# Performance work log

Measured on AMD Instinct MI355X. Metric: run time of the kernel, lower is better.

The kernel has to match this reference:

```python
import jax, jax.numpy as jnp
import numpy as np

D_FEAT = 6
T = 60
H = 64          # hidden_size
N = 8192        # number of stocks (cross-sectional batch)
LRELU_SLOPE = 0.01
BN_EPS = 1e-5


def _gru_layer(x_seq, W_ih, W_hh, b_ih, b_hh):
    """torch-convention GRU layer. x_seq: (N, T, in) -> (N, T, H)."""
    # precompute input projections for all timesteps: (N, T, 3H)
    xw = jnp.einsum('nti,gi->ntg', x_seq, W_ih) + b_ih

    def step(h, xt):
        gh = h @ W_hh.T + b_hh
        xr, xz, xn = jnp.split(xt, 3, axis=-1)
        hr, hz, hn = jnp.split(gh, 3, axis=-1)
        r = jax.nn.sigmoid(xr + hr)
        z = jax.nn.sigmoid(xz + hz)
        n = jnp.tanh(xn + r * hn)
        h_new = (1.0 - z) * n + z * h
        return h_new, h_new

    h0 = jnp.zeros((x_seq.shape[0], H), x_seq.dtype)
    _, ys = jax.lax.scan(step, h0, jnp.swapaxes(xw, 0, 1))  # (T, N, H)
    return jnp.swapaxes(ys, 0, 1)


def _batchnorm(x, w, b):
    # track_running_stats=False -> always batch statistics (biased var)
    m = jnp.mean(x, axis=0)
    v = jnp.var(x, axis=0)
    return (x - m) * jax.lax.rsqrt(v + BN_EPS) * w + b


def setup_inputs() -> dict:
    key = jax.random.key(0)
    ks = jax.random.split(key, 24)
    s = 1.0 / np.sqrt(H)

    def u(k, shape):
        return jax.random.uniform(k, shape, jnp.float32, -s, s)

    inp = {"x": jax.random.normal(ks[0], (N, D_FEAT * T), jnp.float32)}
    in_sizes = [D_FEAT, H]
    for l in range(2):
        inp[f"W_ih_l{l}"] = u(ks[1 + 4 * l], (3 * H, in_sizes[l]))
        inp[f"W_hh_l{l}"] = u(ks[2 + 4 * l], (3 * H, H))
        inp[f"b_ih_l{l}"] = u(ks[3 + 4 * l], (3 * H,))
        inp[f"b_hh_l{l}"] = u(ks[4 + 4 * l], (3 * H,))
    inp["bn1_w"] = 1.0 + 0.1 * jax.random.normal(ks[9], (H,), jnp.float32)
    inp["bn1_b"] = 0.1 * jax.random.normal(ks[10], (H,), jnp.float32)
    inp["fc_w"] = u(ks[11], (H, H))
    inp["fc_b"] = u(ks[12], (H,))
    inp["bn2_w"] = 1.0 + 0.1 * jax.random.normal(ks[13], (H,), jnp.float32)
    inp["bn2_b"] = 0.1 * jax.random.normal(ks[14], (H,), jnp.float32)
    inp["fc_out_w"] = u(ks[15], (1, H))
    inp["fc_out_b"] = u(ks[16], (1,))
    return inp


def reference(x, W_ih_l0, W_hh_l0, b_ih_l0, b_hh_l0,
              W_ih_l1, W_hh_l1, b_ih_l1, b_hh_l1,
              bn1_w, bn1_b, fc_w, fc_b, bn2_w, bn2_b, fc_out_w, fc_out_b):
    n = x.shape[0]
    xs = x.reshape(n, D_FEAT, -1).transpose(0, 2, 1)  # (N, T, d_feat)
    h = _gru_layer(xs, W_ih_l0, W_hh_l0, b_ih_l0, b_hh_l0)
    h = _gru_layer(h, W_ih_l1, W_hh_l1, b_ih_l1, b_hh_l1)
    hidden = h[:, -1, :]                               # (N, H)
    hidden = _batchnorm(hidden, bn1_w, bn1_b)

    # pairwise covariance: E[x_i * y_j] - E[x_i]E[y_j], mean over H.
    # Algebraically (x @ y.T)/H - e_x e_y^T; no O(N^2*H) intermediate.
    e = jnp.mean(hidden, axis=1, keepdims=True)        # (N, 1)
    gamma = hidden @ hidden.T / H - e @ e.T            # (N, N)

    out = gamma @ hidden                               # (N, H)
    out = out @ fc_w.T + fc_b
    out = _batchnorm(out, bn2_w, bn2_b)
    out = jnp.where(out >= 0, out, LRELU_SLOPE * out)  # LeakyReLU(0.01)
    return (out @ fc_out_w.T + fc_out_b).squeeze()
```

## Files before the change

### kernel.cpp

```cpp
#include <hip/hip_runtime.h>
#include <hip/hip_bf16.h>

#define N_ROWS 8192
#define T_STEPS 60
#define DFEAT 6

typedef _Float16 f16x8 __attribute__((ext_vector_type(8)));
typedef float f32x4 __attribute__((ext_vector_type(4)));
typedef float fvec4 __attribute__((ext_vector_type(4)));

#if __has_builtin(__builtin_amdgcn_exp2f)
#define EXP2F(x) __builtin_amdgcn_exp2f(x)
#else
#define EXP2F(x) exp2f(x)
#endif
#define RCPF(x) __builtin_amdgcn_rcpf(x)

#define LOG2E  1.4426950408889634f
#define LOG2E2 2.8853900817779268f

#define MFMA16(a, b, c) __builtin_amdgcn_mfma_f32_16x16x32_f16(a, b, c, 0, 0, 0)

#define LOAD_WS(W, g, kf, SC, DST) do {                                       \
    const float* _p = (W) + ((g)*64 + jcol)*64 + (kf)*32 + rowgrp*8;          \
    fvec4 _v0 = *(const fvec4*)_p;                                            \
    fvec4 _v1 = *(const fvec4*)(_p + 4);                                      \
    f16x8 _f;                                                                 \
    _Pragma("unroll")                                                         \
    for (int _e = 0; _e < 4; ++_e) {                                          \
        _f[_e]     = (_Float16)(_v0[_e] * (SC));                              \
        _f[4 + _e] = (_Float16)(_v1[_e] * (SC));                              \
    }                                                                         \
    DST = _f;                                                                 \
} while (0)

__device__ __forceinline__ int hswz(int row, int col) {
    return row * 64 + (col ^ ((row & 7) << 3));
}

__global__ __launch_bounds__(512, 4)
void gru_fused(const float* __restrict__ x,
               const float* __restrict__ Wih0, const float* __restrict__ Whh0,
               const float* __restrict__ bih0, const float* __restrict__ bhh0,
               const float* __restrict__ Wih1, const float* __restrict__ Whh1,
               const float* __restrict__ bih1, const float* __restrict__ bhh1,
               _Float16* __restrict__ hidden, _Float16* __restrict__ hiddenT)
{
    __shared__ __align__(16) _Float16 h0s[2][1024];
    __shared__ __align__(16) _Float16 h1s[2][1024];
    __shared__ __align__(16) _Float16 xs[T_STEPS][16][8];
    __shared__ __align__(16) _Float16 zx[8];

    const int tid = threadIdx.x;
    const int lane = tid & 63;
    const int wv = tid >> 6;
    const int roleB = wv >> 2;
    const int cg_ = wv & 3;
    const int lrow = lane & 15;
    const int rowgrp = lane >> 4;
    const int jcol = cg_ * 16 + lrow;
    const int rbase = blockIdx.x * 16;

    for (int i = tid; i < 1024; i += 512) {
        h0s[0][i] = (_Float16)0.f; h0s[1][i] = (_Float16)0.f;
        h1s[0][i] = (_Float16)0.f; h1s[1][i] = (_Float16)0.f;
    }
    if (tid < 8) zx[tid] = (_Float16)0.f;
    for (int idx = tid; idx < 16 * T_STEPS; idx += 512) {
        int t = idx >> 4, r = idx & 15;
        const float* xp = x + (long)(rbase + r) * (DFEAT * T_STEPS) + t;
        f16x8 f;
#pragma unroll
        for (int d = 0; d < DFEAT; ++d) f[d] = (_Float16)xp[d * T_STEPS];
        f[6] = (_Float16)0.f; f[7] = (_Float16)0.f;
        *(f16x8*)&xs[t][r][0] = f;
    }

    f16x8 zerof;
#pragma unroll
    for (int e = 0; e < 8; ++e) zerof[e] = (_Float16)0.f;

    f16x8 wg[12];
#pragma unroll
    for (int i = 0; i < 12; ++i) wg[i] = zerof;
    float br, bz, bxn, bhn;
    if (roleB == 0) {
        LOAD_WS(Whh0, 0, 0, LOG2E,  wg[0]);  LOAD_WS(Whh0, 0, 1, LOG2E,  wg[1]);
        LOAD_WS(Whh0, 1, 0, LOG2E,  wg[2]);  LOAD_WS(Whh0, 1, 1, LOG2E,  wg[3]);
        LOAD_WS(Whh0, 2, 0, LOG2E2, wg[4]);  LOAD_WS(Whh0, 2, 1, LOG2E2, wg[5]);
        if (rowgrp == 0) {
#pragma unroll
            for (int g = 0; g < 3; ++g) {
                const float sc = (g == 2) ? LOG2E2 : LOG2E;
                f16x8 f = zerof;
#pragma unroll
                for (int e = 0; e < DFEAT; ++e)
                    f[e] = (_Float16)(Wih0[(g * 64 + jcol) * DFEAT + e] * sc);
                wg[6 + g] = f;
            }
        }
        br  = (bih0[jcol] + bhh0[jcol]) * LOG2E;
        bz  = (bih0[64 + jcol] + bhh0[64 + jcol]) * LOG2E;
        bxn = bih0[128 + jcol] * LOG2E2;
        bhn = bhh0[128 + jcol] * LOG2E2;
    } else {
        LOAD_WS(Wih1, 0, 0, LOG2E,  wg[0]);  LOAD_WS(Wih1, 0, 1, LOG2E,  wg[1]);
        LOAD_WS(Wih1, 1, 0, LOG2E,  wg[2]);  LOAD_WS(Wih1, 1, 1, LOG2E,  wg[3]);
        LOAD_WS(Wih1, 2, 0, LOG2E2, wg[4]);  LOAD_WS(Wih1, 2, 1, LOG2E2, wg[5]);
        LOAD_WS(Whh1, 0, 0, LOG2E,  wg[6]);  LOAD_WS(Whh1, 0, 1, LOG2E,  wg[7]);
        LOAD_WS(Whh1, 1, 0, LOG2E,  wg[8]);  LOAD_WS(Whh1, 1, 1, LOG2E,  wg[9]);
        LOAD_WS(Whh1, 2, 0, LOG2E2, wg[10]); LOAD_WS(Whh1, 2, 1, LOG2E2, wg[11]);
        br  = (bih1[jcol] + bhh1[jcol]) * LOG2E;
        bz  = (bih1[64 + jcol] + bhh1[64 + jcol]) * LOG2E;
        bxn = bih1[128 + jcol] * LOG2E2;
        bhn = bhh1[128 + jcol] * LOG2E2;
    }

    float hreg[4] = {0.f, 0.f, 0.f, 0.f};

    const _Float16* xbase_l = (rowgrp == 0) ? &xs[0][lrow][0] : &zx[0];
    const long xinc = (rowgrp == 0) ? 128 : 0;

    int widx[4];
#pragma unroll
    for (int q = 0; q < 4; ++q) widx[q] = hswz(rowgrp * 4 + q, jcol);
    const int ridx0 = lrow * 64 + ((rowgrp * 8) ^ ((lrow & 7) << 3));
    const int ridx1 = lrow * 64 + ((32 + rowgrp * 8) ^ ((lrow & 7) << 3));

    __syncthreads();

#pragma unroll 1
    for (int tt = 0; tt <= T_STEPS; ++tt) {
        if (roleB == 0) {
            if (tt < T_STEPS) {
                const int rb = (tt + 1) & 1;
                f16x8 hf0 = *(const f16x8*)&h0s[rb][ridx0];
                f16x8 hf1 = *(const f16x8*)&h0s[rb][ridx1];
                f16x8 xf  = *(const f16x8*)(xbase_l + (long)tt * xinc);
                f32x4 accr  = {br, br, br, br};
                f32x4 accz  = {bz, bz, bz, bz};
                f32x4 accxn = {bxn, bxn, bxn, bxn};
                f32x4 acchn = {bhn, bhn, bhn, bhn};
                accr  = MFMA16(xf,  wg[6], accr);
                accr  = MFMA16(hf0, wg[0], accr);
                accr  = MFMA16(hf1, wg[1], accr);
                accz  = MFMA16(xf,  wg[7], accz);
                accz  = MFMA16(hf0, wg[2], accz);
                accz  = MFMA16(hf1, wg[3], accz);
                accxn = MFMA16(xf,  wg[8], accxn);
                acchn = MFMA16(hf0, wg[4], acchn);
                acchn = MFMA16(hf1, wg[5], acchn);
#pragma unroll
                for (int q = 0; q < 4; ++q) {
                    float r = RCPF(1.0f + EXP2F(-accr[q]));
                    float z = RCPF(1.0f + EXP2F(-accz[q]));
                    float v = accxn[q] + r * acchn[q];
                    float n = 2.0f * RCPF(1.0f + EXP2F(-v)) - 1.0f;
                    hreg[q] = n + z * (hreg[q] - n);
                }
                const int wb = tt & 1;
#pragma unroll
                for (int q = 0; q < 4; ++q)
                    h0s[wb][widx[q]] = (_Float16)hreg[q];
            }
        } else {
            if (tt > 0) {
                const int rb0 = (tt + 1) & 1;
                const int rb1 = tt & 1;
                f16x8 xf0 = *(const f16x8*)&h0s[rb0][ridx0];
                f16x8 xf1 = *(const f16x8*)&h0s[rb0][ridx1];
                f16x8 hf0 = *(const f16x8*)&h1s[rb1][ridx0];
                f16x8 hf1 = *(const f16x8*)&h1s[rb1][ridx1];
                f32x4 accr  = {br, br, br, br};
                f32x4 accz  = {bz, bz, bz, bz};
                f32x4 accxn = {bxn, bxn, bxn, bxn};
                f32x4 acchn = {bhn, bhn, bhn, bhn};
                accr  = MFMA16(xf0, wg[0], accr);
                accr  = MFMA16(xf1, wg[1], accr);
                accr  = MFMA16(hf0, wg[6], accr);
                accr  = MFMA16(hf1, wg[7], accr);
                accz  = MFMA16(xf0, wg[2], accz);
                accz  = MFMA16(xf1, wg[3], accz);
                accz  = MFMA16(hf0, wg[8], accz);
                accz  = MFMA16(hf1, wg[9], accz);
                accxn = MFMA16(xf0, wg[4], accxn);
                accxn = MFMA16(xf1, wg[5], accxn);
                acchn = MFMA16(hf0, wg[10], acchn);
                acchn = MFMA16(hf1, wg[11], acchn);
#pragma unroll
                for (int q = 0; q < 4; ++q) {
                    float r = RCPF(1.0f + EXP2F(-accr[q]));
                    float z = RCPF(1.0f + EXP2F(-accz[q]));
                    float v = accxn[q] + r * acchn[q];
                    float n = 2.0f * RCPF(1.0f + EXP2F(-v)) - 1.0f;
                    hreg[q] = n + z * (hreg[q] - n);
                }
                const int wb = (tt + 1) & 1;
#pragma unroll
                for (int q = 0; q < 4; ++q)
                    h1s[wb][widx[q]] = (_Float16)hreg[q];
            }
        }
        __syncthreads();
    }

    if (roleB == 1) {
#pragma unroll
        for (int q = 0; q < 4; ++q) {
            const int row = rbase + rowgrp * 4 + q;
            _Float16 hv = (_Float16)hreg[q];
            hidden[(long)row * 64 + jcol] = hv;
            hiddenT[(long)jcol * N_ROWS + row] = hv;
        }
    }
}

__global__ __launch_bounds__(256)
void gram_kernel(const _Float16* __restrict__ hiddenT,
                 float* __restrict__ Graw, float* __restrict__ colsum)
{
    __shared__ float red[3][64][4];
    const int tid = threadIdx.x;
    const int wv = tid >> 6, lane = tid & 63;
    const int lrow = lane & 15, rg = lane >> 4;
    const int r = blockIdx.x >> 2, c = blockIdx.x & 3;

    const _Float16* pb = hiddenT + (long)(c * 16 + lrow) * N_ROWS + wv * 2048 + rg * 8;
    f32x4 acc[4];
#pragma unroll
    for (int i = 0; i < 4; ++i) acc[i] = (f32x4){0.f, 0.f, 0.f, 0.f};

    if (r < 4) {
        const _Float16* pa = hiddenT + (long)(r * 16 + lrow) * N_ROWS + wv * 2048 + rg * 8;
#pragma unroll 4
        for (int kf = 0; kf < 64; ++kf) {
            f16x8 af = *(const f16x8*)(pa + kf * 32);
            f16x8 bf = *(const f16x8*)(pb + kf * 32);
            acc[kf & 3] = MFMA16(af, bf, acc[kf & 3]);
        }
    } else {
        f16x8 af;
#pragma unroll
        for (int e = 0; e < 8; ++e) af[e] = (lrow == 0) ? (_Float16)1.f : (_Float16)0.f;
#pragma unroll 4
        for (int kf = 0; kf < 64; ++kf) {
            f16x8 bf = *(const f16x8*)(pb + kf * 32);
            acc[kf & 3] = MFMA16(af, bf, acc[kf & 3]);
        }
    }
    f32x4 a0 = acc[0] + acc[1] + acc[2] + acc[3];

    if (wv > 0) {
#pragma unroll
        for (int q = 0; q < 4; ++q) red[wv - 1][lane][q] = a0[q];
    }
    __syncthreads();
    if (wv == 0) {
#pragma unroll
        for (int q = 0; q < 4; ++q)
            a0[q] += red[0][lane][q] + red[1][lane][q] + red[2][lane][q];
        if (r < 4) {
#pragma unroll
            for (int q = 0; q < 4; ++q)
                Graw[(r * 16 + rg * 4 + q) * 64 + c * 16 + lrow] = a0[q];
        } else if (rg == 0) {
            colsum[c * 16 + lrow] = a0[0];
        }
    }
}

__global__ __launch_bounds__(256)
void final_kernel(const _Float16* __restrict__ hidden,
                  const float* __restrict__ Graw, const float* __restrict__ colsum,
                  const float* __restrict__ bn1w, const float* __restrict__ bn1b,
                  const float* __restrict__ fcw,  const float* __restrict__ fcb,
                  const float* __restrict__ bn2w, const float* __restrict__ bn2b,
                  const float* __restrict__ fow,  const float* __restrict__ fob,
                  float* __restrict__ y)
{
    __shared__ float Gbn[64][65];
    __shared__ float Ms[64][65];
    __shared__ _Float16 tile[128][72];
    __shared__ float el[128];
    __shared__ float a1s[64], c1s[64], S1s[64], S1bn[64], s_s[64];
    __shared__ float svs[64], a2s[64], c2s[64], fcs[64], wos[64];
    __shared__ float red[4][64];
    __shared__ float E2s, Esums;

    const int b = blockIdx.x, tid = threadIdx.x;
    const float Nf = (float)N_ROWS;

    if (tid < 64) {
        float S1 = colsum[tid];
        S1s[tid] = S1;
        float m = S1 * (1.0f / Nf);
        float var = Graw[tid * 65] * (1.0f / Nf) - m * m;
        float a = bn1w[tid] * rsqrtf(var + 1e-5f);
        float cc = bn1b[tid] - m * a;
        a1s[tid] = a; c1s[tid] = cc;
        S1bn[tid] = a * S1 + Nf * cc;
    }
    __syncthreads();

    for (int i = tid; i < 4096; i += 256) {
        int j = i >> 6, k = i & 63;
        Gbn[j][k] = a1s[j] * a1s[k] * Graw[i]
                  + a1s[j] * c1s[k] * S1s[j]
                  + c1s[j] * a1s[k] * S1s[k]
                  + Nf * c1s[j] * c1s[k];
    }
    __syncthreads();

    {
        const int k = tid & 63, g = tid >> 6;
        float p = 0.f;
        for (int j = g * 16; j < g * 16 + 16; ++j) p += Gbn[j][k];
        red[g][k] = p;
    }
    __syncthreads();
    if (tid < 64)
        s_s[tid] = (red[0][tid] + red[1][tid] + red[2][tid] + red[3][tid]) * (1.0f / 64.0f);
    __syncthreads();
    if (tid == 0) {
        float e2 = 0.f, es = 0.f;
        for (int k = 0; k < 64; ++k) { e2 += s_s[k]; es += S1bn[k]; }
        E2s = e2 * (1.0f / 64.0f);
        Esums = es * (1.0f / 64.0f);
    }

    for (int i = tid; i < 4096; i += 256) {
        int k = i >> 6, p = i & 63;
        float acc = 0.f;
#pragma unroll 8
        for (int j = 0; j < 64; ++j) acc += Gbn[k][j] * fcw[p * 64 + j];
        Ms[k][p] = acc * (1.0f / 64.0f);
    }
    __syncthreads();

    {
        const int p = tid & 63, g = tid >> 6;
        float pa = 0.f;
        for (int j = g * 16; j < g * 16 + 16; ++j) {
            float gm = 0.f;
#pragma unroll 8
            for (int k = 0; k < 64; ++k) gm += Gbn[j][k] * Ms[k][p];
            pa += Ms[j][p] * gm;
        }
        red[g][p] = pa;
    }
    __syncthreads();

    if (tid < 64) {
        const int p = tid;
        float A = red[0][p] + red[1][p] + red[2][p] + red[3][p];
        float sv = 0.f, B = 0.f, SuS = 0.f;
#pragma unroll 8
        for (int j = 0; j < 64; ++j) {
            sv  += s_s[j] * fcw[p * 64 + j];
            B   += s_s[j] * Ms[j][p];
            SuS += S1bn[j] * Ms[j][p];
        }
        float Su  = SuS - Esums * sv;
        float Su2 = A - 2.0f * sv * B + E2s * sv * sv;
        float f = fcb[p];
        float cs = Su + Nf * f;
        float cq = Su2 + 2.0f * f * Su + Nf * f * f;
        float m2 = cs * (1.0f / Nf);
        float v2 = cq * (1.0f / Nf) - m2 * m2;
        float a = bn2w[p] * rsqrtf(v2 + 1e-5f);
        a2s[p] = a; c2s[p] = bn2b[p] - m2 * a;
        svs[p] = sv; fcs[p] = f; wos[p] = fow[p];
    }
    __syncthreads();

    for (int i = tid; i < 128 * 64; i += 256) {
        int r = i >> 6, cc = i & 63;
        float hv = (float)hidden[(long)(b * 128 + r) * 64 + cc];
        tile[r][cc] = (_Float16)(hv * a1s[cc] + c1s[cc]);
    }
    __syncthreads();
    for (int r = tid; r < 128; r += 256) {
        float s = 0.f;
#pragma unroll 8
        for (int cc = 0; cc < 64; ++cc) s += (float)tile[r][cc];
        el[r] = s * (1.0f / 64.0f);
    }
    __syncthreads();

    const float bo = fob[0];
#pragma unroll 1
    for (int pass = 0; pass < 4; ++pass) {
        const int row = pass * 32 + (tid >> 3);
        const int pg = (tid & 7) << 3;
        float acc[8];
#pragma unroll
        for (int i = 0; i < 8; ++i) acc[i] = 0.f;
#pragma unroll 4
        for (int k = 0; k < 64; ++k) {
            float hv = (float)tile[row][k];
#pragma unroll
            for (int i = 0; i < 8; ++i) acc[i] += hv * Ms[k][pg + i];
        }
        const float ev = el[row];
        float part = 0.f;
#pragma unroll
        for (int i = 0; i < 8; ++i) {
            int p = pg + i;
            float v = acc[i] - ev * svs[p] + fcs[p];
            v = v * a2s[p] + c2s[p];
            v = (v >= 0.f) ? v : 0.01f * v;
            part += v * wos[p];
        }
        part += __shfl_xor(part, 1);
        part += __shfl_xor(part, 2);
        part += __shfl_xor(part, 4);
        if ((tid & 7) == 0) y[b * 128 + row] = part + bo;
    }
}

extern "C" void kernel_launch(void* const* d_in, const int* in_sizes, int n_in,
                              void* d_out, int out_size, void* d_ws, size_t ws_size,
                              hipStream_t stream)
{
    const float* x    = (const float*)d_in[0];
    const float* Wih0 = (const float*)d_in[1];
    const float* Whh0 = (const float*)d_in[2];
    const float* bih0 = (const float*)d_in[3];
    const float* bhh0 = (const float*)d_in[4];
    const float* Wih1 = (const float*)d_in[5];
    const float* Whh1 = (const float*)d_in[6];
    const float* bih1 = (const float*)d_in[7];
    const float* bhh1 = (const float*)d_in[8];
    const float* bn1w = (const float*)d_in[9];
    const float* bn1b = (const float*)d_in[10];
    const float* fcw  = (const float*)d_in[11];
    const float* fcb  = (const float*)d_in[12];
    const float* bn2w = (const float*)d_in[13];
    const float* bn2b = (const float*)d_in[14];
    const float* fow  = (const float*)d_in[15];
    const float* fob  = (const float*)d_in[16];
    float* y = (float*)d_out;

    _Float16* hidden  = (_Float16*)d_ws;
    _Float16* hiddenT = hidden + 524288;
    float* Graw   = (float*)(hidden + 1048576);
    float* colsum = Graw + 4096;

    gru_fused<<<512, 512, 0, stream>>>(x, Wih0, Whh0, bih0, bhh0,
                                       Wih1, Whh1, bih1, bhh1,
                                       hidden, hiddenT);
    gram_kernel<<<24, 256, 0, stream>>>(hiddenT, Graw, colsum);
    final_kernel<<<64, 256, 0, stream>>>(hidden, Graw, colsum, bn1w, bn1b,
                                         fcw, fcb, bn2w, bn2b, fow, fob, y);
}
```

Before: 232.5 us.

## Fold Gram computation into final kernel and raise wave priority around MFMAs

The separate gram_kernel launch is removed. Each of the 64 final_kernel blocks now recomputes the 64x64 Gram matrix and column sums redundantly from hiddenT into shared memory, with one wave per column tile looping over all 8192 rows. This drops a kernel launch and the global round trip for Graw/colsum, but multiplies the Gram work and hiddenT reads 64-fold and serializes a long reduction per block. Separately, s_setprio is raised around the MFMA chains in the GRU recurrence so those waves get issue priority.

```diff
diff --git a/kernel.cpp b/kernel.cpp
--- a/kernel.cpp
+++ b/kernel.cpp
@@ -141,6 +141,7 @@
                 f32x4 accz  = {bz, bz, bz, bz};
                 f32x4 accxn = {bxn, bxn, bxn, bxn};
                 f32x4 acchn = {bhn, bhn, bhn, bhn};
+                __builtin_amdgcn_s_setprio(1);
                 accr  = MFMA16(xf,  wg[6], accr);
                 accr  = MFMA16(hf0, wg[0], accr);
                 accr  = MFMA16(hf1, wg[1], accr);
@@ -150,6 +151,7 @@
                 accxn = MFMA16(xf,  wg[8], accxn);
                 acchn = MFMA16(hf0, wg[4], acchn);
                 acchn = MFMA16(hf1, wg[5], acchn);
+                __builtin_amdgcn_s_setprio(0);
 #pragma unroll
                 for (int q = 0; q < 4; ++q) {
                     float r = RCPF(1.0f + EXP2F(-accr[q]));
@@ -175,6 +177,7 @@
                 f32x4 accz  = {bz, bz, bz, bz};
                 f32x4 accxn = {bxn, bxn, bxn, bxn};
                 f32x4 acchn = {bhn, bhn, bhn, bhn};
+                __builtin_amdgcn_s_setprio(1);
                 accr  = MFMA16(xf0, wg[0], accr);
                 accr  = MFMA16(xf1, wg[1], accr);
                 accr  = MFMA16(hf0, wg[6], accr);
@@ -187,6 +190,7 @@
                 accxn = MFMA16(xf1, wg[5], accxn);
                 acchn = MFMA16(hf0, wg[10], acchn);
                 acchn = MFMA16(hf1, wg[11], acchn);
+                __builtin_amdgcn_s_setprio(0);
 #pragma unroll
                 for (int q = 0; q < 4; ++q) {
                     float r = RCPF(1.0f + EXP2F(-accr[q]));
@@ -216,68 +220,16 @@
 }
 
 __global__ __launch_bounds__(256)
-void gram_kernel(const _Float16* __restrict__ hiddenT,
-                 float* __restrict__ Graw, float* __restrict__ colsum)
-{
-    __shared__ float red[3][64][4];
-    const int tid = threadIdx.x;
-    const int wv = tid >> 6, lane = tid & 63;
-    const int lrow = lane & 15, rg = lane >> 4;
-    const int r = blockIdx.x >> 2, c = blockIdx.x & 3;
-
-    const _Float16* pb = hiddenT + (long)(c * 16 + lrow) * N_ROWS + wv * 2048 + rg * 8;
-    f32x4 acc[4];
-#pragma unroll
-    for (int i = 0; i < 4; ++i) acc[i] = (f32x4){0.f, 0.f, 0.f, 0.f};
-
-    if (r < 4) {
-        const _Float16* pa = hiddenT + (long)(r * 16 + lrow) * N_ROWS + wv * 2048 + rg * 8;
-#pragma unroll 4
-        for (int kf = 0; kf < 64; ++kf) {
-            f16x8 af = *(const f16x8*)(pa + kf * 32);
-            f16x8 bf = *(const f16x8*)(pb + kf * 32);
-            acc[kf & 3] = MFMA16(af, bf, acc[kf & 3]);
-        }
-    } else {
-        f16x8 af;
-#pragma unroll
-        for (int e = 0; e < 8; ++e) af[e] = (lrow == 0) ? (_Float16)1.f : (_Float16)0.f;
-#pragma unroll 4
-        for (int kf = 0; kf < 64; ++kf) {
-            f16x8 bf = *(const f16x8*)(pb + kf * 32);
-            acc[kf & 3] = MFMA16(af, bf, acc[kf & 3]);
-        }
-    }
-    f32x4 a0 = acc[0] + acc[1] + acc[2] + acc[3];
-
-    if (wv > 0) {
-#pragma unroll
-        for (int q = 0; q < 4; ++q) red[wv - 1][lane][q] = a0[q];
-    }
-    __syncthreads();
-    if (wv == 0) {
-#pragma unroll
-        for (int q = 0; q < 4; ++q)
-            a0[q] += red[0][lane][q] + red[1][lane][q] + red[2][lane][q];
-        if (r < 4) {
-#pragma unroll
-            for (int q = 0; q < 4; ++q)
-                Graw[(r * 16 + rg * 4 + q) * 64 + c * 16 + lrow] = a0[q];
-        } else if (rg == 0) {
-            colsum[c * 16 + lrow] = a0[0];
-        }
-    }
-}
-
-__global__ __launch_bounds__(256)
 void final_kernel(const _Float16* __restrict__ hidden,
-                  const float* __restrict__ Graw, const float* __restrict__ colsum,
+                  const _Float16* __restrict__ hiddenT,
                   const float* __restrict__ bn1w, const float* __restrict__ bn1b,
                   const float* __restrict__ fcw,  const float* __restrict__ fcb,
                   const float* __restrict__ bn2w, const float* __restrict__ bn2b,
                   const float* __restrict__ fow,  const float* __restrict__ fob,
                   float* __restrict__ y)
 {
+    __shared__ float Graw_s[64][65];
+    __shared__ float colsum_s[64];
     __shared__ float Gbn[64][65];
     __shared__ float Ms[64][65];
     __shared__ _Float16 tile[128][72];
@@ -288,13 +240,54 @@
     __shared__ float E2s, Esums;
 
     const int b = blockIdx.x, tid = threadIdx.x;
+    const int wv = tid >> 6, lane = tid & 63;
+    const int lrow = lane & 15, rg = lane >> 4;
     const float Nf = (float)N_ROWS;
 
+    {
+        const int c = wv;
+        const _Float16* pb = hiddenT + (long)(c * 16 + lrow) * N_ROWS + rg * 8;
+#pragma unroll 1
+        for (int r = 0; r < 5; ++r) {
+            f32x4 acc[4];
+#pragma unroll
+            for (int i = 0; i < 4; ++i) acc[i] = (f32x4){0.f, 0.f, 0.f, 0.f};
+            if (r < 4) {
+                const _Float16* pa = hiddenT + (long)(r * 16 + lrow) * N_ROWS + rg * 8;
+#pragma unroll 4
+                for (int kf = 0; kf < 256; ++kf) {
+                    f16x8 af = *(const f16x8*)(pa + kf * 32);
+                    f16x8 bf = *(const f16x8*)(pb + kf * 32);
+                    acc[kf & 3] = MFMA16(af, bf, acc[kf & 3]);
+                }
+            } else {
+                f16x8 af;
+#pragma unroll
+                for (int e = 0; e < 8; ++e)
+                    af[e] = (lrow == 0) ? (_Float16)1.f : (_Float16)0.f;
+#pragma unroll 4
+                for (int kf = 0; kf < 256; ++kf) {
+                    f16x8 bf = *(const f16x8*)(pb + kf * 32);
+                    acc[kf & 3] = MFMA16(af, bf, acc[kf & 3]);
+                }
+            }
+            f32x4 a0 = acc[0] + acc[1] + acc[2] + acc[3];
+            if (r < 4) {
+#pragma unroll
+                for (int q = 0; q < 4; ++q)
+                    Graw_s[r * 16 + rg * 4 + q][c * 16 + lrow] = a0[q];
+            } else if (rg == 0) {
+                colsum_s[c * 16 + lrow] = a0[0];
+            }
+        }
+    }
+    __syncthreads();
+
     if (tid < 64) {
-        float S1 = colsum[tid];
+        float S1 = colsum_s[tid];
         S1s[tid] = S1;
         float m = S1 * (1.0f / Nf);
-        float var = Graw[tid * 65] * (1.0f / Nf) - m * m;
+        float var = Graw_s[tid][tid] * (1.0f / Nf) - m * m;
         float a = bn1w[tid] * rsqrtf(var + 1e-5f);
         float cc = bn1b[tid] - m * a;
         a1s[tid] = a; c1s[tid] = cc;
@@ -304,7 +297,7 @@
 
     for (int i = tid; i < 4096; i += 256) {
         int j = i >> 6, k = i & 63;
-        Gbn[j][k] = a1s[j] * a1s[k] * Graw[i]
+        Gbn[j][k] = a1s[j] * a1s[k] * Graw_s[j][k]
                   + a1s[j] * c1s[k] * S1s[j]
                   + c1s[j] * a1s[k] * S1s[k]
                   + Nf * c1s[j] * c1s[k];
@@ -443,13 +436,10 @@
 
     _Float16* hidden  = (_Float16*)d_ws;
     _Float16* hiddenT = hidden + 524288;
-    float* Graw   = (float*)(hidden + 1048576);
-    float* colsum = Graw + 4096;
 
     gru_fused<<<512, 512, 0, stream>>>(x, Wih0, Whh0, bih0, bhh0,
                                        Wih1, Whh1, bih1, bhh1,
                                        hidden, hiddenT);
-    gram_kernel<<<24, 256, 0, stream>>>(hiddenT, Graw, colsum);
-    final_kernel<<<64, 256, 0, stream>>>(hidden, Graw, colsum, bn1w, bn1b,
+    final_kernel<<<64, 256, 0, stream>>>(hidden, hiddenT, bn1w, bn1b,
                                          fcw, fcb, bn2w, bn2b, fow, fob, y);
 }
```

After: 466.4 us. +100.6%, slower.
